# Performance work log

Hardware: AMD Instinct MI355X
Metric: run time of the kernel (lower is better)

The kernel has to match this reference:

```python
import jax, jax.numpy as jnp
import numpy as np

N_NODES = 50000
N_EDGES = 800000
F_IN = 128
HIDDEN = 128
N_CLASSES = 40


def setup_inputs() -> dict:
    key = jax.random.key(0)
    ks = jax.random.split(key, 8)
    x = jax.random.normal(ks[0], (N_NODES, F_IN), dtype=jnp.float32)
    edge_index = jax.random.randint(ks[1], (2, N_EDGES), 0, N_NODES, dtype=jnp.int32)
    s_in = 1.0 / np.sqrt(F_IN)
    s_h = 1.0 / np.sqrt(HIDDEN)
    W1_l = jax.random.normal(ks[2], (F_IN, HIDDEN), jnp.float32) * s_in
    W1_r = jax.random.normal(ks[3], (F_IN, HIDDEN), jnp.float32) * s_in
    b1 = jnp.zeros((HIDDEN,), jnp.float32)
    W2_l = jax.random.normal(ks[4], (HIDDEN, N_CLASSES), jnp.float32) * s_h
    W2_r = jax.random.normal(ks[5], (HIDDEN, N_CLASSES), jnp.float32) * s_h
    b2 = jnp.zeros((N_CLASSES,), jnp.float32)
    return {"x": x, "edge_index": edge_index, "W1_l": W1_l, "W1_r": W1_r,
            "b1": b1, "W2_l": W2_l, "W2_r": W2_r, "b2": b2}


def _sage_conv(x, src, dst, W_l, W_r, b):
    # mean-aggregate neighbor features at dst, then linear transform + root weight
    msg = x[src]                                                  # [E, d] gather
    agg = jax.ops.segment_sum(msg, dst, num_segments=N_NODES)     # [N, d] scatter-add
    deg = jax.ops.segment_sum(jnp.ones((src.shape[0],), x.dtype), dst,
                              num_segments=N_NODES)
    agg = agg / jnp.maximum(deg, 1.0)[:, None]                    # mean aggregation
    return agg @ W_l + x @ W_r + b


def reference(x, edge_index, W1_l, W1_r, b1, W2_l, W2_r, b2):
    src, dst = edge_index[0], edge_index[1]
    h = jax.nn.relu(_sage_conv(x, src, dst, W1_l, W1_r, b1))
    # F.dropout(p=0.5, training=self.training) -> identity in eval mode
    out = jax.nn.relu(_sage_conv(h, src, dst, W2_l, W2_r, b2))
    return jax.nn.log_softmax(out, axis=-1)
```

## Files before the change

kernel.cpp:

```cpp
#include <hip/hip_runtime.h>

#define N_NODES 50000
#define N_EDGES 800000
#define F_IN 128
#define HIDDEN 128
#define N_CLASSES 40

#define NBUCKET 391
#define BUCKET_CAP 4096
#define BINA_CHUNK 2048
#define BINA_NBLK 391
#define PREP_ITEMS (N_NODES * 32 + 128 * 256 + 80 * 128)
#define PREP_NBLK (PREP_ITEMS / 256)

#define OFF_RS     0
#define OFF_BCNT   50004
#define OFF_INVDEG 100004
#define OFF_SRCS   150004
#define OFF_XB     950004
#define OFF_BINS   7350004
#define OFF_PB     7350004
#define OFF_Q      8350004
#define OFF_WT1    10550004
#define OFF_WT2    10566388

typedef short bf16x8 __attribute__((ext_vector_type(8)));
typedef float f32x4 __attribute__((ext_vector_type(4)));
typedef unsigned short u16x8 __attribute__((ext_vector_type(8)));

static __device__ __forceinline__ unsigned short f2bf(float f) {
  unsigned int u = __builtin_bit_cast(unsigned int, f);
  u = (u + 0x7fffu + ((u >> 16) & 1u)) >> 16;
  return (unsigned short)u;
}
static __device__ __forceinline__ float bf2f(unsigned short s) {
  unsigned int u = ((unsigned int)s) << 16;
  return __builtin_bit_cast(float, u);
}

__global__ __launch_bounds__(256) void k_binA_prep(
    const int* __restrict__ src, const int* __restrict__ dst,
    int* __restrict__ bcnt, int* __restrict__ bins,
    const float* __restrict__ x, const float* __restrict__ W1l,
    const float* __restrict__ W1r, const float* __restrict__ W2l,
    const float* __restrict__ W2r, unsigned short* __restrict__ xb,
    unsigned short* __restrict__ Wt1, unsigned short* __restrict__ Wt2) {
  if (blockIdx.x >= BINA_NBLK) {
    int idx = (blockIdx.x - BINA_NBLK) * 256 + threadIdx.x;
    if (idx < N_NODES * 32) {
      int row = idx >> 5, c4 = (idx & 31) << 2;
      const float4 v = *(const float4*)(x + (size_t)row * F_IN + c4);
      ushort4 o;
      o.x = f2bf(v.x); o.y = f2bf(v.y); o.z = f2bf(v.z); o.w = f2bf(v.w);
      *(ushort4*)(xb + (size_t)row * 128 + c4) = o;
      return;
    }
    idx -= N_NODES * 32;
    if (idx < 128 * 256) {
      int n = idx >> 8, k = idx & 255;
      float v = (k < 128) ? W1l[(size_t)k * 128 + n]
                          : W1r[(size_t)(k - 128) * 128 + n];
      Wt1[(size_t)n * 256 + k] = f2bf(v);
    } else if (idx < 128 * 256 + 80 * 128) {
      int j = idx - 128 * 256;
      int n = j >> 7, k = j & 127;
      float v = (n < 40) ? W2l[(size_t)k * 40 + n]
                         : W2r[(size_t)k * 40 + (n - 40)];
      Wt2[(size_t)n * 128 + k] = f2bf(v);
    }
    return;
  }
  __shared__ int cnt[NBUCKET];
  __shared__ int excl[NBUCKET];
  __shared__ int cursor[NBUCKET];
  __shared__ int bbase[NBUCKET];
  __shared__ int sc[256];
  __shared__ int stage[BINA_CHUNK];
  __shared__ unsigned short bkt[BINA_CHUNK];
  int t = threadIdx.x;
  int e0 = blockIdx.x * BINA_CHUNK;
  int ne = N_EDGES - e0;
  if (ne > BINA_CHUNK) ne = BINA_CHUNK;
  for (int i = t; i < NBUCKET; i += 256) cnt[i] = 0;
  __syncthreads();
  for (int i = t; i < ne; i += 256) atomicAdd(&cnt[dst[e0 + i] >> 7], 1);
  __syncthreads();
  int a = (2 * t < NBUCKET) ? cnt[2 * t] : 0;
  int b2_ = (2 * t + 1 < NBUCKET) ? cnt[2 * t + 1] : 0;
  int s = a + b2_;
  sc[t] = s;
  __syncthreads();
  for (int off = 1; off < 256; off <<= 1) {
    int add = (t >= off) ? sc[t - off] : 0;
    __syncthreads();
    sc[t] += add;
    __syncthreads();
  }
  int pbase = sc[t] - s;
  if (2 * t < NBUCKET) { excl[2 * t] = pbase; cursor[2 * t] = pbase; }
  if (2 * t + 1 < NBUCKET) {
    excl[2 * t + 1] = pbase + a;
    cursor[2 * t + 1] = pbase + a;
  }
  for (int i = t; i < NBUCKET; i += 256)
    bbase[i] = atomicAdd(&bcnt[i], cnt[i]);
  __syncthreads();
  for (int i = t; i < ne; i += 256) {
    int d = dst[e0 + i];
    int sv = src[e0 + i];
    int b = d >> 7;
    int pos = atomicAdd(&cursor[b], 1);
    stage[pos] = ((d & 127) << 16) | sv;
    bkt[pos] = (unsigned short)b;
  }
  __syncthreads();
  for (int i = t; i < ne; i += 256) {
    int b = bkt[i];
    bins[(size_t)b * BUCKET_CAP + bbase[b] + (i - excl[b])] = stage[i];
  }
}

__global__ __launch_bounds__(256) void k_binB(
    const int* __restrict__ bcnt, const int* __restrict__ bins,
    int* __restrict__ rs, int* __restrict__ srcs,
    float* __restrict__ invdeg) {
  __shared__ int sc[256];
  __shared__ int hist[128];
  __shared__ int cursor[128];
  int b = blockIdx.x;
  int t = threadIdx.x;
  int v = 0;
  if (t < b) v += bcnt[t];
  if (t + 256 < b) v += bcnt[t + 256];
  sc[t] = v;
  __syncthreads();
  for (int off = 128; off; off >>= 1) {
    if (t < off) sc[t] += sc[t + off];
    __syncthreads();
  }
  int base = sc[0];
  int cnt = bcnt[b];
  const int* bb = bins + (size_t)b * BUCKET_CAP;
  if (t < 128) hist[t] = 0;
  __syncthreads();
  for (int i = t; i < cnt; i += 256) atomicAdd(&hist[bb[i] >> 16], 1);
  __syncthreads();
  int c = (t < 128) ? hist[t] : 0;
  sc[t] = c;
  __syncthreads();
  for (int off = 1; off < 128; off <<= 1) {
    int add = (t >= off) ? sc[t - off] : 0;
    __syncthreads();
    sc[t] += add;
    __syncthreads();
  }
  int lexcl = sc[t] - c;
  int node = b * 128 + t;
  if (t < 128 && node < N_NODES) {
    rs[node] = base + lexcl;
    invdeg[node] = 1.0f / (float)(c > 1 ? c : 1);
  }
  if (b == 0 && t == 0) rs[N_NODES] = N_EDGES;
  if (t < 128) cursor[t] = lexcl;
  __syncthreads();
  for (int i = t; i < cnt; i += 256) {
    int v2 = bb[i];
    int pos = atomicAdd(&cursor[v2 >> 16], 1);
    srcs[base + pos] = v2 & 0xFFFF;
  }
}

__global__ __launch_bounds__(256) void k_fused(
    const unsigned short* __restrict__ xb, const int* __restrict__ rs,
    const int* __restrict__ srcs, const float* __restrict__ invdeg,
    const unsigned short* __restrict__ Wt1, const unsigned short* __restrict__ Wt2,
    const float* __restrict__ b1, const float* __restrict__ b2,
    unsigned short* __restrict__ pb, float* __restrict__ q) {
  __shared__ unsigned short as[32 * 264];
  __shared__ unsigned short hs[32 * 132];
  int w = threadIdx.x >> 6, lane = threadIdx.x & 63;
  int t = threadIdx.x;
  int row0 = blockIdx.x * 32;

  for (int chunk = t; chunk < 32 * 16; chunk += 256) {
    int lrow = chunk >> 4, c8 = (chunk & 15) * 8;
    int grow = row0 + lrow;
    if (grow >= N_NODES) grow = N_NODES - 1;
    u16x8 v = *(const u16x8*)(xb + (size_t)grow * 128 + c8);
    *(u16x8*)(as + lrow * 264 + 128 + c8) = v;
  }

  int slot = lane >> 3, li = lane & 7;
  for (int j = 0; j < 8; j++) {
    int lrow = w * 8 + j;
    int node = row0 + lrow;
    int beg = 0, end = 0;
    if (node < N_NODES) { beg = rs[node]; end = rs[node + 1]; }
    float acc[16];
#pragma unroll
    for (int k = 0; k < 16; k++) acc[k] = 0.f;
    for (int i = beg + slot; i < end; i += 8) {
      int s = srcs[i];
      const unsigned short* rp = xb + (size_t)s * 128 + li * 8;
      u16x8 v0 = *(const u16x8*)rp;
      u16x8 v1 = *(const u16x8*)(rp + 64);
#pragma unroll
      for (int k = 0; k < 8; k++) {
        acc[k] += bf2f(v0[k]);
        acc[8 + k] += bf2f(v1[k]);
      }
    }
#pragma unroll
    for (int off = 8; off <= 32; off <<= 1)
#pragma unroll
      for (int k = 0; k < 16; k++) acc[k] += __shfl_xor(acc[k], off, 64);
    if (slot == 0) {
      int nidx = (node < N_NODES) ? node : 0;
      float inv = invdeg[nidx];
      u16x8 o0, o1;
#pragma unroll
      for (int k = 0; k < 8; k++) {
        o0[k] = f2bf(acc[k] * inv);
        o1[k] = f2bf(acc[8 + k] * inv);
      }
      *(u16x8*)(as + lrow * 264 + li * 8) = o0;
      *(u16x8*)(as + lrow * 264 + 64 + li * 8) = o1;
    }
  }
  __syncthreads();

  int r = lane & 15, quad = lane >> 4;
  const unsigned short* Bp = Wt1 + (size_t)(w * 32 + r) * 256 + quad * 8;
  const unsigned short* A0 = as + r * 264 + quad * 8;
  const unsigned short* A1 = as + (16 + r) * 264 + quad * 8;
  f32x4 acc1[2][2];
#pragma unroll
  for (int nn = 0; nn < 2; nn++)
#pragma unroll
    for (int rt = 0; rt < 2; rt++) acc1[nn][rt] = (f32x4){0.f, 0.f, 0.f, 0.f};
#pragma unroll
  for (int k0 = 0; k0 < 256; k0 += 32) {
    bf16x8 a0 = *(const bf16x8*)(A0 + k0);
    bf16x8 a1 = *(const bf16x8*)(A1 + k0);
#pragma unroll
    for (int nn = 0; nn < 2; nn++) {
      bf16x8 bv = *(const bf16x8*)(Bp + (size_t)nn * 16 * 256 + k0);
      acc1[nn][0] = __builtin_amdgcn_mfma_f32_16x16x32_bf16(a0, bv, acc1[nn][0], 0, 0, 0);
      acc1[nn][1] = __builtin_amdgcn_mfma_f32_16x16x32_bf16(a1, bv, acc1[nn][1], 0, 0, 0);
    }
  }
  __syncthreads();
#pragma unroll
  for (int nn = 0; nn < 2; nn++) {
    int col = (w * 2 + nn) * 16 + r;
    float bias = b1[col];
#pragma unroll
    for (int rt = 0; rt < 2; rt++)
#pragma unroll
      for (int reg = 0; reg < 4; reg++)
        hs[(rt * 16 + quad * 4 + reg) * 132 + col] =
            f2bf(fmaxf(acc1[nn][rt][reg] + bias, 0.f));
  }
  __syncthreads();

  int rt2 = w & 1, ng = w >> 1;
  int nbeg = ng ? 3 : 0;
  int ncnt = ng ? 2 : 3;
  const unsigned short* hrow = hs + (rt2 * 16 + r) * 132 + quad * 8;
  const unsigned short* Bp2 = Wt2 + (size_t)(nbeg * 16 + r) * 128 + quad * 8;
  f32x4 acc2[3];
#pragma unroll
  for (int j = 0; j < 3; j++) acc2[j] = (f32x4){0.f, 0.f, 0.f, 0.f};
#pragma unroll
  for (int k0 = 0; k0 < 128; k0 += 32) {
    ushort4 h0 = *(const ushort4*)(hrow + k0);
    ushort4 h1 = *(const ushort4*)(hrow + k0 + 4);
    bf16x8 af;
    af[0] = (short)h0.x; af[1] = (short)h0.y; af[2] = (short)h0.z; af[3] = (short)h0.w;
    af[4] = (short)h1.x; af[5] = (short)h1.y; af[6] = (short)h1.z; af[7] = (short)h1.w;
#pragma unroll
    for (int j = 0; j < 3; j++) {
      if (j < ncnt) {
        bf16x8 bv = *(const bf16x8*)(Bp2 + (size_t)j * 16 * 128 + k0);
        acc2[j] = __builtin_amdgcn_mfma_f32_16x16x32_bf16(af, bv, acc2[j], 0, 0, 0);
      }
    }
  }
  int crow0 = row0 + rt2 * 16 + quad * 4;
#pragma unroll
  for (int j = 0; j < 3; j++) {
    if (j < ncnt) {
      int col = (nbeg + j) * 16 + r;
#pragma unroll
      for (int reg = 0; reg < 4; reg++) {
        int row = crow0 + reg;
        if (row < N_NODES) {
          float v = acc2[j][reg];
          if (col < N_CLASSES)
            pb[(size_t)row * 40 + col] = f2bf(v);
          else
            q[(size_t)row * N_CLASSES + (col - N_CLASSES)] = v + b2[col - N_CLASSES];
        }
      }
    }
  }
}

__global__ __launch_bounds__(256) void k_final(
    const unsigned short* __restrict__ pb, const float* __restrict__ q,
    const int* __restrict__ rs, const int* __restrict__ srcs,
    const float* __restrict__ invdeg, float* __restrict__ out) {
  int node = blockIdx.x * 4 + (threadIdx.x >> 6);
  int lane = threadIdx.x & 63;
  int slot = lane >> 3, li = lane & 7;
  if (node >= N_NODES) return;
  bool valid = li < 5;
  int beg = rs[node], end = rs[node + 1];
  float acc[8];
#pragma unroll
  for (int j = 0; j < 8; j++) acc[j] = 0.f;
  for (int i = beg + slot; i < end; i += 8) {
    int s = srcs[i];
    if (valid) {
      u16x8 v = *(const u16x8*)(pb + (size_t)s * 40 + li * 8);
#pragma unroll
      for (int j = 0; j < 8; j++) acc[j] += bf2f(v[j]);
    }
  }
#pragma unroll
  for (int off = 8; off <= 32; off <<= 1)
#pragma unroll
    for (int j = 0; j < 8; j++) acc[j] += __shfl_xor(acc[j], off, 64);
  float inv = invdeg[node];
  float v[8];
  float m = -1e30f;
  if (valid) {
    const float* qr = q + (size_t)node * N_CLASSES + li * 8;
    float4 q0 = *(const float4*)qr;
    float4 q1 = *(const float4*)(qr + 4);
    v[0] = fmaxf(acc[0] * inv + q0.x, 0.f);
    v[1] = fmaxf(acc[1] * inv + q0.y, 0.f);
    v[2] = fmaxf(acc[2] * inv + q0.z, 0.f);
    v[3] = fmaxf(acc[3] * inv + q0.w, 0.f);
    v[4] = fmaxf(acc[4] * inv + q1.x, 0.f);
    v[5] = fmaxf(acc[5] * inv + q1.y, 0.f);
    v[6] = fmaxf(acc[6] * inv + q1.z, 0.f);
    v[7] = fmaxf(acc[7] * inv + q1.w, 0.f);
#pragma unroll
    for (int j = 0; j < 8; j++) m = fmaxf(m, v[j]);
  }
#pragma unroll
  for (int off = 1; off <= 4; off <<= 1) m = fmaxf(m, __shfl_xor(m, off, 8));
  float ssum = 0.f;
  if (valid) {
#pragma unroll
    for (int j = 0; j < 8; j++) ssum += __expf(v[j] - m);
  }
#pragma unroll
  for (int off = 1; off <= 4; off <<= 1) ssum += __shfl_xor(ssum, off, 8);
  float lse = __logf(ssum) + m;
  if (slot == 0 && valid) {
    float* orow = out + (size_t)node * N_CLASSES + li * 8;
    *(float4*)orow = make_float4(v[0] - lse, v[1] - lse, v[2] - lse, v[3] - lse);
    *(float4*)(orow + 4) =
        make_float4(v[4] - lse, v[5] - lse, v[6] - lse, v[7] - lse);
  }
}

extern "C" void kernel_launch(void* const* d_in, const int* in_sizes, int n_in,
                              void* d_out, int out_size, void* d_ws,
                              size_t ws_size, hipStream_t stream) {
  const float* x   = (const float*)d_in[0];
  const int*   ei  = (const int*)d_in[1];
  const int*   src = ei;
  const int*   dst = ei + N_EDGES;
  const float* W1l = (const float*)d_in[2];
  const float* W1r = (const float*)d_in[3];
  const float* b1  = (const float*)d_in[4];
  const float* W2l = (const float*)d_in[5];
  const float* W2r = (const float*)d_in[6];
  const float* b2  = (const float*)d_in[7];
  float* out = (float*)d_out;

  float* wsf = (float*)d_ws;
  int*   rs     = (int*)wsf + OFF_RS;
  int*   bcnt   = (int*)wsf + OFF_BCNT;
  float* invdeg = wsf + OFF_INVDEG;
  int*   srcs   = (int*)wsf + OFF_SRCS;
  unsigned short* xb  = (unsigned short*)(wsf + OFF_XB);
  unsigned short* pb  = (unsigned short*)(wsf + OFF_PB);
  unsigned short* Wt1 = (unsigned short*)(wsf + OFF_WT1);
  unsigned short* Wt2 = (unsigned short*)(wsf + OFF_WT2);
  int*   bins   = (int*)wsf + OFF_BINS;
  float* q = wsf + OFF_Q;

  hipMemsetAsync(bcnt, 0, NBUCKET * sizeof(int), stream);

  k_binA_prep<<<BINA_NBLK + PREP_NBLK, 256, 0, stream>>>(
      src, dst, bcnt, bins, x, W1l, W1r, W2l, W2r, xb, Wt1, Wt2);
  k_binB<<<NBUCKET, 256, 0, stream>>>(bcnt, bins, rs, srcs, invdeg);
  k_fused<<<(N_NODES + 31) / 32, 256, 0, stream>>>(
      xb, rs, srcs, invdeg, Wt1, Wt2, b1, b2, pb, q);
  k_final<<<(N_NODES + 3) / 4, 256, 0, stream>>>(pb, q, rs, srcs, invdeg, out);
}
```

Measured before the change: 212.7 us.

## Widen fused block to 64 rows, 512 threads, and unroll neighbor gathers by two

The fused layer-1 kernel now handles 64 rows per block with 8 waves. Each wave computes one 16-column slice of the first GEMM across all four row tiles, so every B-fragment load is reused four times and one barrier is removed. Both neighbor-aggregation loops, in the fused and final kernels, now issue two independent row gathers per iteration to keep more memory loads in flight. The cost is more LDS per block and more registers per thread, which may lower occupancy, and fewer blocks for load balancing.

```diff
diff --git a/kernel.cpp b/kernel.cpp
--- a/kernel.cpp
+++ b/kernel.cpp
@@ -170,19 +170,19 @@
   }
 }
 
-__global__ __launch_bounds__(256) void k_fused(
+__global__ __launch_bounds__(512) void k_fused(
     const unsigned short* __restrict__ xb, const int* __restrict__ rs,
     const int* __restrict__ srcs, const float* __restrict__ invdeg,
     const unsigned short* __restrict__ Wt1, const unsigned short* __restrict__ Wt2,
     const float* __restrict__ b1, const float* __restrict__ b2,
     unsigned short* __restrict__ pb, float* __restrict__ q) {
-  __shared__ unsigned short as[32 * 264];
-  __shared__ unsigned short hs[32 * 132];
+  __shared__ unsigned short as[64 * 264];
+  __shared__ unsigned short hs[64 * 132];
   int w = threadIdx.x >> 6, lane = threadIdx.x & 63;
   int t = threadIdx.x;
-  int row0 = blockIdx.x * 32;
-
-  for (int chunk = t; chunk < 32 * 16; chunk += 256) {
+  int row0 = blockIdx.x * 64;
+
+  for (int chunk = t; chunk < 64 * 16; chunk += 512) {
     int lrow = chunk >> 4, c8 = (chunk & 15) * 8;
     int grow = row0 + lrow;
     if (grow >= N_NODES) grow = N_NODES - 1;
@@ -199,15 +199,30 @@
     float acc[16];
 #pragma unroll
     for (int k = 0; k < 16; k++) acc[k] = 0.f;
-    for (int i = beg + slot; i < end; i += 8) {
-      int s = srcs[i];
-      const unsigned short* rp = xb + (size_t)s * 128 + li * 8;
-      u16x8 v0 = *(const u16x8*)rp;
-      u16x8 v1 = *(const u16x8*)(rp + 64);
+    int i = beg + slot;
+    for (; i + 8 < end; i += 16) {
+      int s0 = srcs[i], s1 = srcs[i + 8];
+      const unsigned short* rp0 = xb + (size_t)s0 * 128 + li * 8;
+      const unsigned short* rp1 = xb + (size_t)s1 * 128 + li * 8;
+      u16x8 a0 = *(const u16x8*)rp0;
+      u16x8 a1 = *(const u16x8*)(rp0 + 64);
+      u16x8 c0 = *(const u16x8*)rp1;
+      u16x8 c1 = *(const u16x8*)(rp1 + 64);
 #pragma unroll
       for (int k = 0; k < 8; k++) {
-        acc[k] += bf2f(v0[k]);
-        acc[8 + k] += bf2f(v1[k]);
+        acc[k] += bf2f(a0[k]) + bf2f(c0[k]);
+        acc[8 + k] += bf2f(a1[k]) + bf2f(c1[k]);
+      }
+    }
+    if (i < end) {
+      int s0 = srcs[i];
+      const unsigned short* rp0 = xb + (size_t)s0 * 128 + li * 8;
+      u16x8 a0 = *(const u16x8*)rp0;
+      u16x8 a1 = *(const u16x8*)(rp0 + 64);
+#pragma unroll
+      for (int k = 0; k < 8; k++) {
+        acc[k] += bf2f(a0[k]);
+        acc[8 + k] += bf2f(a1[k]);
       }
     }
 #pragma unroll
@@ -230,40 +245,32 @@
   __syncthreads();
 
   int r = lane & 15, quad = lane >> 4;
-  const unsigned short* Bp = Wt1 + (size_t)(w * 32 + r) * 256 + quad * 8;
-  const unsigned short* A0 = as + r * 264 + quad * 8;
-  const unsigned short* A1 = as + (16 + r) * 264 + quad * 8;
-  f32x4 acc1[2][2];
-#pragma unroll
-  for (int nn = 0; nn < 2; nn++)
-#pragma unroll
-    for (int rt = 0; rt < 2; rt++) acc1[nn][rt] = (f32x4){0.f, 0.f, 0.f, 0.f};
+  const unsigned short* Bp = Wt1 + (size_t)(w * 16 + r) * 256 + quad * 8;
+  f32x4 acc1[4];
+#pragma unroll
+  for (int rt = 0; rt < 4; rt++) acc1[rt] = (f32x4){0.f, 0.f, 0.f, 0.f};
 #pragma unroll
   for (int k0 = 0; k0 < 256; k0 += 32) {
-    bf16x8 a0 = *(const bf16x8*)(A0 + k0);
-    bf16x8 a1 = *(const bf16x8*)(A1 + k0);
-#pragma unroll
-    for (int nn = 0; nn < 2; nn++) {
-      bf16x8 bv = *(const bf16x8*)(Bp + (size_t)nn * 16 * 256 + k0);
-      acc1[nn][0] = __builtin_amdgcn_mfma_f32_16x16x32_bf16(a0, bv, acc1[nn][0], 0, 0, 0);
-      acc1[nn][1] = __builtin_amdgcn_mfma_f32_16x16x32_bf16(a1, bv, acc1[nn][1], 0, 0, 0);
-    }
-  }
-  __syncthreads();
-#pragma unroll
-  for (int nn = 0; nn < 2; nn++) {
-    int col = (w * 2 + nn) * 16 + r;
+    bf16x8 bv = *(const bf16x8*)(Bp + k0);
+#pragma unroll
+    for (int rt = 0; rt < 4; rt++) {
+      bf16x8 av = *(const bf16x8*)(as + (rt * 16 + r) * 264 + quad * 8 + k0);
+      acc1[rt] = __builtin_amdgcn_mfma_f32_16x16x32_bf16(av, bv, acc1[rt], 0, 0, 0);
+    }
+  }
+  {
+    int col = w * 16 + r;
     float bias = b1[col];
 #pragma unroll
-    for (int rt = 0; rt < 2; rt++)
+    for (int rt = 0; rt < 4; rt++)
 #pragma unroll
       for (int reg = 0; reg < 4; reg++)
         hs[(rt * 16 + quad * 4 + reg) * 132 + col] =
-            f2bf(fmaxf(acc1[nn][rt][reg] + bias, 0.f));
-  }
-  __syncthreads();
-
-  int rt2 = w & 1, ng = w >> 1;
+            f2bf(fmaxf(acc1[rt][reg] + bias, 0.f));
+  }
+  __syncthreads();
+
+  int rt2 = w >> 1, ng = w & 1;
   int nbeg = ng ? 3 : 0;
   int ncnt = ng ? 2 : 3;
   const unsigned short* hrow = hs + (rt2 * 16 + r) * 132 + quad * 8;
@@ -319,12 +326,22 @@
   float acc[8];
 #pragma unroll
   for (int j = 0; j < 8; j++) acc[j] = 0.f;
-  for (int i = beg + slot; i < end; i += 8) {
-    int s = srcs[i];
+  int i = beg + slot;
+  for (; i + 8 < end; i += 16) {
+    int s0 = srcs[i], s1 = srcs[i + 8];
     if (valid) {
-      u16x8 v = *(const u16x8*)(pb + (size_t)s * 40 + li * 8);
-#pragma unroll
-      for (int j = 0; j < 8; j++) acc[j] += bf2f(v[j]);
+      u16x8 v0 = *(const u16x8*)(pb + (size_t)s0 * 40 + li * 8);
+      u16x8 v1 = *(const u16x8*)(pb + (size_t)s1 * 40 + li * 8);
+#pragma unroll
+      for (int j = 0; j < 8; j++) acc[j] += bf2f(v0[j]) + bf2f(v1[j]);
+    }
+  }
+  if (i < end) {
+    int s0 = srcs[i];
+    if (valid) {
+      u16x8 v0 = *(const u16x8*)(pb + (size_t)s0 * 40 + li * 8);
+#pragma unroll
+      for (int j = 0; j < 8; j++) acc[j] += bf2f(v0[j]);
     }
   }
 #pragma unroll
@@ -399,7 +416,7 @@
   k_binA_prep<<<BINA_NBLK + PREP_NBLK, 256, 0, stream>>>(
       src, dst, bcnt, bins, x, W1l, W1r, W2l, W2r, xb, Wt1, Wt2);
   k_binB<<<NBUCKET, 256, 0, stream>>>(bcnt, bins, rs, srcs, invdeg);
-  k_fused<<<(N_NODES + 31) / 32, 256, 0, stream>>>(
+  k_fused<<<(N_NODES + 63) / 64, 512, 0, stream>>>(
       xb, rs, srcs, invdeg, Wt1, Wt2, b1, b2, pb, q);
   k_final<<<(N_NODES + 3) / 4, 256, 0, stream>>>(pb, q, rs, srcs, invdeg, out);
 }
```

Measured after the change: 208.1 us. 1.02x faster.
